# Performance work log

Measured on AMD Instinct MI355X. Metric: run time of the kernel, lower is better.

Reference implementation:

```python
import jax, jax.numpy as jnp
import numpy as np

E_EDGES = 100000   # number of original edges (edge tokens)
M_PAIRS = 1000000  # number of edge-edge (line-graph) pairs
IN_DIM = 128
H = 8   # num_heads
D = 16  # out_dim per head


def setup_inputs() -> dict:
    key = jax.random.key(0)
    ks = jax.random.split(key, 8)
    edge_attr = jax.random.normal(ks[0], (E_EDGES, IN_DIM), dtype=jnp.float32)
    edge_edge_index = jax.random.randint(ks[1], (2, M_PAIRS), 0, E_EDGES, dtype=jnp.int64)
    s = 1.0 / np.sqrt(IN_DIM)  # xavier-ish scale
    Wq = jax.random.normal(ks[2], (IN_DIM, H * D), dtype=jnp.float32) * s
    Wk = jax.random.normal(ks[3], (IN_DIM, H * D), dtype=jnp.float32) * s
    Wv = jax.random.normal(ks[4], (IN_DIM, H * D), dtype=jnp.float32) * s
    bq = jnp.zeros((H * D,), dtype=jnp.float32)
    bk = jnp.zeros((H * D,), dtype=jnp.float32)
    bv = jnp.zeros((H * D,), dtype=jnp.float32)
    Aw = jax.random.normal(ks[5], (D, H), dtype=jnp.float32) * (1.0 / np.sqrt(D))
    return {"edge_attr": edge_attr, "edge_edge_index": edge_edge_index,
            "Wq": Wq, "bq": bq, "Wk": Wk, "bk": bk, "Wv": Wv, "bv": bv, "Aw": Aw}


def reference(edge_attr, edge_edge_index, Wq, bq, Wk, bk, Wv, bv, Aw):
    E = edge_attr.shape[0]
    # Q/K/V projections, reshaped to [E, H, D]
    Qh = (edge_attr @ Wq + bq).reshape(E, H, D)
    Kh = (edge_attr @ Wk + bk).reshape(E, H, D)
    Vh = (edge_attr @ Wv + bv).reshape(E, H, D)
    src = edge_edge_index[0]
    dst = edge_edge_index[1]
    # gather + additive score over edge-edge pairs: [M, H, D]
    score_vec = Kh[src] + Qh[dst]  # act = Identity
    # einsum 'ehd,dhc->ehc' with c=1 -> [M, H]
    raw_attn = jnp.einsum('mhd,dh->mh', score_vec, Aw)
    # segment softmax grouped by destination edge
    mx = jax.ops.segment_max(raw_attn, dst, num_segments=E)  # [E, H]
    ex = jnp.exp(raw_attn - mx[dst])
    denom = jax.ops.segment_sum(ex, dst, num_segments=E)[dst] + 1e-16
    attn = ex / denom  # [M, H]; dropout p=0 -> identity
    # weighted scatter-add aggregation
    msg = Vh[src] * attn[..., None]  # [M, H, D]
    edge_out = jax.ops.segment_sum(msg, dst, num_segments=E)  # [E, H, D]
    return edge_out
```

## Files before the change

### kernel.cpp

```cpp
#include <hip/hip_runtime.h>
#include <math.h>

static constexpr int E = 100000;
static constexpr int M = 1000000;
static constexpr int NBE = (E + 255) / 256;
static constexpr int NBM = (M + 255) / 256;
static constexpr int NBP = (E + 63) / 64;
static constexpr int NBM4 = (M + 1023) / 1024;

#define O_FLAG   0
#define O_WEFF   512
#define O_BKEFF  4608
#define O_BSWZ   5120
#define O_COUNTS 38400
#define O_OFFS   438784
#define O_BSUM   838784
#define O_BSUM2  840832
#define O_BINOFF 842880
#define O_GBIN   843904
#define O_ORDER  1245312
#define O_POS    1645312
#define O_CSR    5645312
#define O_KS     9645312
#define O_VH     12845312
#define WS_NEEDED (O_VH + (size_t)E * 128 * 2)

typedef float f32x4 __attribute__((ext_vector_type(4)));
typedef short s16x8 __attribute__((ext_vector_type(8)));

__device__ __forceinline__ unsigned short f2bf(float f) {
    unsigned u = __float_as_uint(f);
    u += 0x7fffu + ((u >> 16) & 1u);
    return (unsigned short)(u >> 16);
}
__device__ __forceinline__ float bflo(unsigned u) { return __uint_as_float(u << 16); }
__device__ __forceinline__ float bfhi(unsigned u) { return __uint_as_float(u & 0xffff0000u); }

__device__ __forceinline__ int weswz(int k) { return (k ^ ((k >> 3) & 3)) << 3; }

__global__ void k_prep(const float* __restrict__ Wk, const float* __restrict__ bk,
                       const float* __restrict__ Aw, const float* __restrict__ Wv,
                       const int* __restrict__ idx32, int* __restrict__ flag,
                       float* __restrict__ weff, float* __restrict__ bkeff,
                       unsigned short* __restrict__ Bswz) {
    int bid = blockIdx.x, t = threadIdx.x;
    if (bid == 0) {
        if (t < 128) {
            for (int h = 0; h < 8; h++) {
                float s = 0.f;
                for (int d = 0; d < 16; d++) s += Wk[t * 128 + h * 16 + d] * Aw[d * 8 + h];
                weff[t * 8 + h] = s;
            }
            if (t < 8) {
                float s = 0.f;
                for (int d = 0; d < 16; d++) s += bk[t * 16 + d] * Aw[d * 8 + t];
                bkeff[t] = s;
            }
        }
        return;
    }
    if (bid == 1) {
        if (t == 0) {
            int z = 0;
            for (int i = 0; i < 64; i++) z += (idx32[2 * i + 1] == 0) ? 1 : 0;
            *flag = (z == 64) ? 1 : 0;
        }
        return;
    }
    int p = (bid - 2) * 256 + t;
    int f = p >> 6, lane = p & 63;
    int c = f >> 3, tt = f & 7;
    int quad = lane >> 4, nn = lane & 15;
#pragma unroll
    for (int j = 0; j < 8; j++) {
        int k = c * 32 + quad * 8 + j;
        Bswz[p * 8 + j] = f2bf(Wv[k * 128 + tt * 16 + nn]);
    }
}

__global__ __launch_bounds__(256) void k_cp(
    const void* __restrict__ idx, const int* __restrict__ flagp,
    int* __restrict__ counts, int* __restrict__ pos,
    const float* __restrict__ A, const short* __restrict__ Bswz,
    const float* __restrict__ bv, const float* __restrict__ weff,
    const float* __restrict__ bkeff, unsigned short* __restrict__ Vh,
    float* __restrict__ ksb) {
    int bid = blockIdx.x, t = threadIdx.x;
    int r = bid % 5;
    if (r < 2) {
        int cid = (bid / 5) * 2 + r;
        if (cid >= NBM4) return;
        int base = cid * 1024 + t;
        int m0 = base, m1 = base + 256, m2 = base + 512, m3 = base + 768;
        int d0 = 0, d1 = 0, d2 = 0, d3 = 0;
        if (*flagp) {
            const long long* p = (const long long*)idx;
            if (m0 < M) d0 = (int)p[M + m0];
            if (m1 < M) d1 = (int)p[M + m1];
            if (m2 < M) d2 = (int)p[M + m2];
            if (m3 < M) d3 = (int)p[M + m3];
        } else {
            const int* p = (const int*)idx;
            if (m0 < M) d0 = p[M + m0];
            if (m1 < M) d1 = p[M + m1];
            if (m2 < M) d2 = p[M + m2];
            if (m3 < M) d3 = p[M + m3];
        }
        if (m0 < M) pos[m0] = atomicAdd(&counts[d0], 1);
        if (m1 < M) pos[m1] = atomicAdd(&counts[d1], 1);
        if (m2 < M) pos[m2] = atomicAdd(&counts[d2], 1);
        if (m3 < M) pos[m3] = atomicAdd(&counts[d3], 1);
        return;
    }
    int pid = (bid / 5) * 3 + (r - 2);
    if (pid >= NBP) return;

    __shared__ float we[1024];
    {
        int k = t >> 1;
        int off = weswz(k) + ((t & 1) << 2);
        *(float4*)&we[off] = ((const float4*)weff)[t];
    }
    __syncthreads();

    int lane = t & 63, wid = t >> 6;
    int rowbase = pid * 64 + wid * 16;
    int quad = lane >> 4, nn = lane & 15;
    int m = rowbase + nn;
    int mc = (m < E) ? m : (E - 1);

    f32x4 acc[8];
#pragma unroll
    for (int tt = 0; tt < 8; tt++) acc[tt] = (f32x4){0.f, 0.f, 0.f, 0.f};
    float p[8];
#pragma unroll
    for (int h = 0; h < 8; h++) p[h] = 0.f;

#pragma unroll
    for (int c = 0; c < 4; c++) {
        const float4* ap = (const float4*)(A + (size_t)mc * 128 + c * 32 + quad * 8);
        float4 f0 = ap[0], f1 = ap[1];
        float a[8] = {f0.x, f0.y, f0.z, f0.w, f1.x, f1.y, f1.z, f1.w};
#pragma unroll
        for (int j = 0; j < 8; j++) {
            int k = c * 32 + quad * 8 + j;
            int kb = weswz(k);
            float4 w0 = *(const float4*)&we[kb];
            float4 w1 = *(const float4*)&we[kb + 4];
            p[0] += a[j] * w0.x; p[1] += a[j] * w0.y;
            p[2] += a[j] * w0.z; p[3] += a[j] * w0.w;
            p[4] += a[j] * w1.x; p[5] += a[j] * w1.y;
            p[6] += a[j] * w1.z; p[7] += a[j] * w1.w;
        }
        s16x8 afrag;
#pragma unroll
        for (int j = 0; j < 8; j++) afrag[j] = (short)f2bf(a[j]);
#pragma unroll
        for (int tt = 0; tt < 8; tt++) {
            s16x8 bfrag = *(const s16x8*)(Bswz + (((c * 8 + tt) * 64 + lane) << 3));
            acc[tt] = __builtin_amdgcn_mfma_f32_16x16x32_bf16(afrag, bfrag, acc[tt], 0, 0, 0);
        }
    }
#pragma unroll
    for (int off = 16; off <= 32; off <<= 1)
#pragma unroll
        for (int h = 0; h < 8; h++) p[h] += __shfl_xor(p[h], off, 64);
    if (quad == 0 && m < E) {
        float4* op = (float4*)(ksb + (size_t)m * 8);
        op[0] = make_float4(p[0] + bkeff[0], p[1] + bkeff[1], p[2] + bkeff[2], p[3] + bkeff[3]);
        op[1] = make_float4(p[4] + bkeff[4], p[5] + bkeff[5], p[6] + bkeff[6], p[7] + bkeff[7]);
    }
#pragma unroll
    for (int tt = 0; tt < 8; tt++) {
        float bvc = bv[tt * 16 + nn];
#pragma unroll
        for (int rr = 0; rr < 4; rr++) {
            int row = rowbase + quad * 4 + rr;
            if (row < E)
                Vh[(size_t)row * 128 + tt * 16 + nn] = f2bf(acc[tt][rr] + bvc);
        }
    }
}

__global__ void k_scanA(int* __restrict__ counts, int* __restrict__ offs,
                        int* __restrict__ bsum, int* __restrict__ gbin) {
    __shared__ int sm[256];
    __shared__ int lh[256];
    __shared__ int bb[256];
    int tid = threadIdx.x;
    int i = blockIdx.x * 256 + tid;
    int v = (i < E) ? counts[i] : 0;
    int n = v > 255 ? 255 : v;
    lh[tid] = 0;
    sm[tid] = v;
    __syncthreads();
    int lr = 0;
    if (i < E) lr = atomicAdd(&lh[n], 1);
    for (int off = 1; off < 256; off <<= 1) {
        int add = (tid >= off) ? sm[tid - off] : 0;
        __syncthreads();
        sm[tid] += add;
        __syncthreads();
    }
    if (i < E) offs[i] = sm[tid] - v;
    if (tid == 255) bsum[blockIdx.x] = sm[255];
    int cnt = lh[tid];
    if (cnt > 0) bb[tid] = atomicAdd(&gbin[tid * 8], cnt);
    __syncthreads();
    if (i < E) counts[i] = ((bb[n] + lr) << 8) | n;
}

__global__ void k_scanB2(const int* __restrict__ bsum, const int* __restrict__ gbin,
                         int* __restrict__ bsum2, int* __restrict__ binoff, int nb) {
    __shared__ int sm[512];
    __shared__ int s2[256];
    int tid = threadIdx.x;
    int v = (tid < nb) ? bsum[tid] : 0;
    sm[tid] = v;
    __syncthreads();
    for (int off = 1; off < 512; off <<= 1) {
        int add = (tid >= off) ? sm[tid - off] : 0;
        __syncthreads();
        sm[tid] += add;
        __syncthreads();
    }
    bsum2[tid] = sm[tid] - v;
    int bv = 0;
    if (tid < 256) { bv = gbin[(255 - tid) * 8]; s2[tid] = bv; }
    __syncthreads();
    for (int off = 1; off < 256; off <<= 1) {
        int add = (tid < 256 && tid >= off) ? s2[tid - off] : 0;
        __syncthreads();
        if (tid < 256) s2[tid] += add;
        __syncthreads();
    }
    if (tid < 256) binoff[255 - tid] = s2[tid] - bv;
}

__global__ void k_fill(const void* __restrict__ idx, const int* __restrict__ flagp,
                       const int* __restrict__ offs, const int* __restrict__ bsum2,
                       const int* __restrict__ pos, int* __restrict__ csr,
                       const int* __restrict__ counts, const int* __restrict__ binoff,
                       int* __restrict__ order) {
    int bid = blockIdx.x, t = threadIdx.x;
    if (bid < NBM) {
        int m = bid * 256 + t;
        if (m >= M) return;
        int s, d;
        if (*flagp) {
            const long long* p = (const long long*)idx;
            s = (int)p[m]; d = (int)p[M + m];
        } else {
            const int* p = (const int*)idx;
            s = p[m]; d = p[M + m];
        }
        csr[offs[d] + bsum2[d >> 8] + pos[m]] = s;
        return;
    }
    int i = (bid - NBM) * 256 + t;
    if (i >= E) return;
    int v = counts[i];
    order[binoff[v & 255] + (v >> 8)] = i;
}

#define ROWL(p, sidx, cond) \
    if (cond) { \
        k##p = ksb[(size_t)(sidx) * 8 + h]; \
        const uint4* vp_ = (const uint4*)(Vh + (size_t)(sidx) * 128 + (h << 4)); \
        a##p = vp_[0]; b##p = vp_[1]; \
    }

#define CONS(kk, aa, bb) { \
    float w_ = __expf(kk); \
    l += w_; \
    acc[0]  += bflo(aa.x) * w_; acc[1]  += bfhi(aa.x) * w_; \
    acc[2]  += bflo(aa.y) * w_; acc[3]  += bfhi(aa.y) * w_; \
    acc[4]  += bflo(aa.z) * w_; acc[5]  += bfhi(aa.z) * w_; \
    acc[6]  += bflo(aa.w) * w_; acc[7]  += bfhi(aa.w) * w_; \
    acc[8]  += bflo(bb.x) * w_; acc[9]  += bfhi(bb.x) * w_; \
    acc[10] += bflo(bb.y) * w_; acc[11] += bfhi(bb.y) * w_; \
    acc[12] += bflo(bb.z) * w_; acc[13] += bfhi(bb.z) * w_; \
    acc[14] += bflo(bb.w) * w_; acc[15] += bfhi(bb.w) * w_; \
}

__global__ __launch_bounds__(256) void k_seg(
    const float* __restrict__ ksb, const unsigned short* __restrict__ Vh,
    const int* __restrict__ offs, const int* __restrict__ bsum2,
    const int* __restrict__ csr, const int* __restrict__ order,
    float* __restrict__ out) {
    int t = threadIdx.x;
    int h = t & 7;
    int g = blockIdx.x * 32 + (t >> 3);
    int seg = order[g];
    int beg = offs[seg] + bsum2[seg >> 8];
    int end = (seg + 1 < E) ? (offs[seg + 1] + bsum2[(seg + 1) >> 8]) : M;
    int n = end - beg;

    float acc[16];
#pragma unroll
    for (int j = 0; j < 16; j++) acc[j] = 0.f;
    float l = 0.f;

    if (n > 0) {
        int s0 = 0, s1 = 0, s2 = 0, s3 = 0, t0 = 0, t1 = 0, t2 = 0, t3 = 0;
        float k0 = 0, k1 = 0, k2 = 0, k3 = 0;
        uint4 a0 = {}, b0 = {}, a1 = {}, b1 = {}, a2 = {}, b2 = {}, a3 = {}, b3 = {};
        s0 = csr[beg];
        if (n > 1) s1 = csr[beg + 1];
        if (n > 2) s2 = csr[beg + 2];
        if (n > 3) s3 = csr[beg + 3];
        ROWL(0, s0, true)
        ROWL(1, s1, n > 1)
        ROWL(2, s2, n > 2)
        ROWL(3, s3, n > 3)
        if (n > 4) t0 = csr[beg + 4];
        if (n > 5) t1 = csr[beg + 5];
        if (n > 6) t2 = csr[beg + 6];
        if (n > 7) t3 = csr[beg + 7];
        int i = 0;
        while (i + 4 <= n) {
            CONS(k0, a0, b0) ROWL(0, t0, i + 4 < n) if (i + 8 < n)  t0 = csr[beg + i + 8];
            CONS(k1, a1, b1) ROWL(1, t1, i + 5 < n) if (i + 9 < n)  t1 = csr[beg + i + 9];
            CONS(k2, a2, b2) ROWL(2, t2, i + 6 < n) if (i + 10 < n) t2 = csr[beg + i + 10];
            CONS(k3, a3, b3) ROWL(3, t3, i + 7 < n) if (i + 11 < n) t3 = csr[beg + i + 11];
            i += 4;
        }
        if (i < n) { CONS(k0, a0, b0) i++; }
        if (i < n) { CONS(k1, a1, b1) i++; }
        if (i < n) { CONS(k2, a2, b2) }
    }
    float inv = 1.0f / (l + 1e-16f);
    float4* op = (float4*)(out + (size_t)seg * 128 + h * 16);
#pragma unroll
    for (int j = 0; j < 4; j++)
        op[j] = make_float4(acc[4 * j] * inv, acc[4 * j + 1] * inv,
                            acc[4 * j + 2] * inv, acc[4 * j + 3] * inv);
}

extern "C" void kernel_launch(void* const* d_in, const int* in_sizes, int n_in,
                              void* d_out, int out_size, void* d_ws, size_t ws_size,
                              hipStream_t stream) {
    const float* edge_attr = (const float*)d_in[0];
    const void*  eei       = d_in[1];
    const float* Wk = (const float*)d_in[4];
    const float* bk = (const float*)d_in[5];
    const float* Wv = (const float*)d_in[6];
    const float* bv = (const float*)d_in[7];
    const float* Aw = (const float*)d_in[8];
    float* out = (float*)d_out;

    if (ws_size < WS_NEEDED) return;

    char* ws = (char*)d_ws;
    int*   flag   = (int*)(ws + O_FLAG);
    float* weff   = (float*)(ws + O_WEFF);
    float* bkeff  = (float*)(ws + O_BKEFF);
    unsigned short* Bswz = (unsigned short*)(ws + O_BSWZ);
    int*   counts = (int*)(ws + O_COUNTS);
    int*   offs   = (int*)(ws + O_OFFS);
    int*   bsum   = (int*)(ws + O_BSUM);
    int*   bsum2  = (int*)(ws + O_BSUM2);
    int*   binoff = (int*)(ws + O_BINOFF);
    int*   gbin   = (int*)(ws + O_GBIN);
    int*   order  = (int*)(ws + O_ORDER);
    int*   pos    = (int*)(ws + O_POS);
    int*   csr    = (int*)(ws + O_CSR);
    float* ksb    = (float*)(ws + O_KS);
    unsigned short* Vh = (unsigned short*)(ws + O_VH);

    hipMemsetAsync(counts, 0, E * sizeof(int), stream);
    hipMemsetAsync(gbin, 0, 256 * 8 * sizeof(int), stream);
    k_prep<<<10, 256, 0, stream>>>(Wk, bk, Aw, Wv, (const int*)eei,
                                   flag, weff, bkeff, Bswz);
    k_cp<<<5 * 521, 256, 0, stream>>>(eei, flag, counts, pos, edge_attr,
                                      (const short*)Bswz, bv, weff, bkeff, Vh, ksb);
    k_scanA<<<NBE, 256, 0, stream>>>(counts, offs, bsum, gbin);
    k_scanB2<<<1, 512, 0, stream>>>(bsum, gbin, bsum2, binoff, NBE);
    k_fill<<<NBM + NBE, 256, 0, stream>>>(eei, flag, offs, bsum2, pos, csr,
                                          counts, binoff, order);
    k_seg<<<E / 32, 256, 0, stream>>>(ksb, Vh, offs, bsum2, csr, order, out);
}
```

Before: 257.6 us.

## Pad histogram counters, fold memsets into prep kernel, precompute exp weights

Pads the per-destination atomic counters to a 4-int stride so concurrent atomics on neighbouring destinations hit different 16-byte slots. Replaces the two memset calls by zeroing counts and gbin inside the prep kernel, which removes launch overhead. Moves the exp of the per-source key score into the projection kernel, so the segment kernel reads precomputed weights and skips one exp per pair. In exchange, the counts array is four times larger and its reads in the scan and fill kernels become strided. The softmax also stays without max subtraction, as before, which can overflow for large scores.

```diff
diff --git a/kernel.cpp b/kernel.cpp
--- a/kernel.cpp
+++ b/kernel.cpp
@@ -7,22 +7,23 @@
 static constexpr int NBM = (M + 255) / 256;
 static constexpr int NBP = (E + 63) / 64;
 static constexpr int NBM4 = (M + 1023) / 1024;
+static constexpr int CSTR = 4;
 
 #define O_FLAG   0
 #define O_WEFF   512
 #define O_BKEFF  4608
 #define O_BSWZ   5120
 #define O_COUNTS 38400
-#define O_OFFS   438784
-#define O_BSUM   838784
-#define O_BSUM2  840832
-#define O_BINOFF 842880
-#define O_GBIN   843904
-#define O_ORDER  1245312
-#define O_POS    1645312
-#define O_CSR    5645312
-#define O_KS     9645312
-#define O_VH     12845312
+#define O_OFFS   1640960
+#define O_BSUM   2040960
+#define O_BSUM2  2043008
+#define O_BINOFF 2045056
+#define O_GBIN   2046080
+#define O_ORDER  2054272
+#define O_POS    2454272
+#define O_CSR    6454272
+#define O_WS     10454272
+#define O_VH     13654272
 #define WS_NEEDED (O_VH + (size_t)E * 128 * 2)
 
 typedef float f32x4 __attribute__((ext_vector_type(4)));
@@ -42,9 +43,14 @@
                        const float* __restrict__ Aw, const float* __restrict__ Wv,
                        const int* __restrict__ idx32, int* __restrict__ flag,
                        float* __restrict__ weff, float* __restrict__ bkeff,
-                       unsigned short* __restrict__ Bswz) {
+                       unsigned short* __restrict__ Bswz, uint4* __restrict__ countsz,
+                       uint4* __restrict__ gbinz) {
     int bid = blockIdx.x, t = threadIdx.x;
-    if (bid == 0) {
+    if (bid < NBE) {
+        countsz[bid * 256 + t] = make_uint4(0, 0, 0, 0);
+        return;
+    }
+    if (bid == NBE) {
         if (t < 128) {
             for (int h = 0; h < 8; h++) {
                 float s = 0.f;
@@ -59,7 +65,9 @@
         }
         return;
     }
-    if (bid == 1) {
+    if (bid == NBE + 1) {
+        gbinz[t * 2] = make_uint4(0, 0, 0, 0);
+        gbinz[t * 2 + 1] = make_uint4(0, 0, 0, 0);
         if (t == 0) {
             int z = 0;
             for (int i = 0; i < 64; i++) z += (idx32[2 * i + 1] == 0) ? 1 : 0;
@@ -67,7 +75,7 @@
         }
         return;
     }
-    int p = (bid - 2) * 256 + t;
+    int p = (bid - (NBE + 2)) * 256 + t;
     int f = p >> 6, lane = p & 63;
     int c = f >> 3, tt = f & 7;
     int quad = lane >> 4, nn = lane & 15;
@@ -84,7 +92,7 @@
     const float* __restrict__ A, const short* __restrict__ Bswz,
     const float* __restrict__ bv, const float* __restrict__ weff,
     const float* __restrict__ bkeff, unsigned short* __restrict__ Vh,
-    float* __restrict__ ksb) {
+    float* __restrict__ wsb) {
     int bid = blockIdx.x, t = threadIdx.x;
     int r = bid % 5;
     if (r < 2) {
@@ -106,10 +114,10 @@
             if (m2 < M) d2 = p[M + m2];
             if (m3 < M) d3 = p[M + m3];
         }
-        if (m0 < M) pos[m0] = atomicAdd(&counts[d0], 1);
-        if (m1 < M) pos[m1] = atomicAdd(&counts[d1], 1);
-        if (m2 < M) pos[m2] = atomicAdd(&counts[d2], 1);
-        if (m3 < M) pos[m3] = atomicAdd(&counts[d3], 1);
+        if (m0 < M) pos[m0] = atomicAdd(&counts[d0 * CSTR], 1);
+        if (m1 < M) pos[m1] = atomicAdd(&counts[d1 * CSTR], 1);
+        if (m2 < M) pos[m2] = atomicAdd(&counts[d2 * CSTR], 1);
+        if (m3 < M) pos[m3] = atomicAdd(&counts[d3 * CSTR], 1);
         return;
     }
     int pid = (bid / 5) * 3 + (r - 2);
@@ -166,9 +174,11 @@
 #pragma unroll
         for (int h = 0; h < 8; h++) p[h] += __shfl_xor(p[h], off, 64);
     if (quad == 0 && m < E) {
-        float4* op = (float4*)(ksb + (size_t)m * 8);
-        op[0] = make_float4(p[0] + bkeff[0], p[1] + bkeff[1], p[2] + bkeff[2], p[3] + bkeff[3]);
-        op[1] = make_float4(p[4] + bkeff[4], p[5] + bkeff[5], p[6] + bkeff[6], p[7] + bkeff[7]);
+        float4* op = (float4*)(wsb + (size_t)m * 8);
+        op[0] = make_float4(__expf(p[0] + bkeff[0]), __expf(p[1] + bkeff[1]),
+                            __expf(p[2] + bkeff[2]), __expf(p[3] + bkeff[3]));
+        op[1] = make_float4(__expf(p[4] + bkeff[4]), __expf(p[5] + bkeff[5]),
+                            __expf(p[6] + bkeff[6]), __expf(p[7] + bkeff[7]));
     }
 #pragma unroll
     for (int tt = 0; tt < 8; tt++) {
@@ -189,7 +199,7 @@
     __shared__ int bb[256];
     int tid = threadIdx.x;
     int i = blockIdx.x * 256 + tid;
-    int v = (i < E) ? counts[i] : 0;
+    int v = (i < E) ? counts[i * CSTR] : 0;
     int n = v > 255 ? 255 : v;
     lh[tid] = 0;
     sm[tid] = v;
@@ -207,7 +217,7 @@
     int cnt = lh[tid];
     if (cnt > 0) bb[tid] = atomicAdd(&gbin[tid * 8], cnt);
     __syncthreads();
-    if (i < E) counts[i] = ((bb[n] + lr) << 8) | n;
+    if (i < E) counts[i * CSTR] = ((bb[n] + lr) << 8) | n;
 }
 
 __global__ void k_scanB2(const int* __restrict__ bsum, const int* __restrict__ gbin,
@@ -259,19 +269,19 @@
     }
     int i = (bid - NBM) * 256 + t;
     if (i >= E) return;
-    int v = counts[i];
+    int v = counts[i * CSTR];
     order[binoff[v & 255] + (v >> 8)] = i;
 }
 
 #define ROWL(p, sidx, cond) \
     if (cond) { \
-        k##p = ksb[(size_t)(sidx) * 8 + h]; \
+        k##p = wsb[(size_t)(sidx) * 8 + h]; \
         const uint4* vp_ = (const uint4*)(Vh + (size_t)(sidx) * 128 + (h << 4)); \
         a##p = vp_[0]; b##p = vp_[1]; \
     }
 
 #define CONS(kk, aa, bb) { \
-    float w_ = __expf(kk); \
+    float w_ = kk; \
     l += w_; \
     acc[0]  += bflo(aa.x) * w_; acc[1]  += bfhi(aa.x) * w_; \
     acc[2]  += bflo(aa.y) * w_; acc[3]  += bfhi(aa.y) * w_; \
@@ -284,7 +294,7 @@
 }
 
 __global__ __launch_bounds__(256) void k_seg(
-    const float* __restrict__ ksb, const unsigned short* __restrict__ Vh,
+    const float* __restrict__ wsb, const unsigned short* __restrict__ Vh,
     const int* __restrict__ offs, const int* __restrict__ bsum2,
     const int* __restrict__ csr, const int* __restrict__ order,
     float* __restrict__ out) {
@@ -365,18 +375,17 @@
     int*   order  = (int*)(ws + O_ORDER);
     int*   pos    = (int*)(ws + O_POS);
     int*   csr    = (int*)(ws + O_CSR);
-    float* ksb    = (float*)(ws + O_KS);
+    float* wsb    = (float*)(ws + O_WS);
     unsigned short* Vh = (unsigned short*)(ws + O_VH);
 
-    hipMemsetAsync(counts, 0, E * sizeof(int), stream);
-    hipMemsetAsync(gbin, 0, 256 * 8 * sizeof(int), stream);
-    k_prep<<<10, 256, 0, stream>>>(Wk, bk, Aw, Wv, (const int*)eei,
-                                   flag, weff, bkeff, Bswz);
+    k_prep<<<NBE + 10, 256, 0, stream>>>(Wk, bk, Aw, Wv, (const int*)eei, flag,
+                                         weff, bkeff, Bswz, (uint4*)counts,
+                                         (uint4*)gbin);
     k_cp<<<5 * 521, 256, 0, stream>>>(eei, flag, counts, pos, edge_attr,
-                                      (const short*)Bswz, bv, weff, bkeff, Vh, ksb);
+                                      (const short*)Bswz, bv, weff, bkeff, Vh, wsb);
     k_scanA<<<NBE, 256, 0, stream>>>(counts, offs, bsum, gbin);
     k_scanB2<<<1, 512, 0, stream>>>(bsum, gbin, bsum2, binoff, NBE);
     k_fill<<<NBM + NBE, 256, 0, stream>>>(eei, flag, offs, bsum2, pos, csr,
                                           counts, binoff, order);
-    k_seg<<<E / 32, 256, 0, stream>>>(ksb, Vh, offs, bsum2, csr, order, out);
-}
+    k_seg<<<E / 32, 256, 0, stream>>>(wsb, Vh, offs, bsum2, csr, order, out);
+}
```

New measurement: 252.0 us. -2.1%, faster.

## Fold memsets into prep kernel, split count/projection kernels, precompute exp weights

Applied to the files above, without the earlier changes.

The two memsets are replaced by zeroing blocks inside the prep kernel, and the weff computation is spread across a full block using shared Aw. The interleaved count+projection kernel is split into two separate launches. The exp of the per-source key score is computed once per edge in the projection kernel instead of once per pair in the segment kernel, removing about a million exp calls. The split adds a kernel launch and loses the overlap between the atomic counting and the MFMA projection.

```diff
diff --git a/kernel.cpp b/kernel.cpp
--- a/kernel.cpp
+++ b/kernel.cpp
@@ -7,6 +7,7 @@
 static constexpr int NBM = (M + 255) / 256;
 static constexpr int NBP = (E + 63) / 64;
 static constexpr int NBM4 = (M + 1023) / 1024;
+static constexpr int NZC = (E / 4 + 255) / 256;
 
 #define O_FLAG   0
 #define O_WEFF   512
@@ -18,11 +19,11 @@
 #define O_BSUM2  840832
 #define O_BINOFF 842880
 #define O_GBIN   843904
-#define O_ORDER  1245312
-#define O_POS    1645312
-#define O_CSR    5645312
-#define O_KS     9645312
-#define O_VH     12845312
+#define O_ORDER  852096
+#define O_POS    1252096
+#define O_CSR    5252096
+#define O_WS     9252096
+#define O_VH     12452096
 #define WS_NEEDED (O_VH + (size_t)E * 128 * 2)
 
 typedef float f32x4 __attribute__((ext_vector_type(4)));
@@ -42,32 +43,45 @@
                        const float* __restrict__ Aw, const float* __restrict__ Wv,
                        const int* __restrict__ idx32, int* __restrict__ flag,
                        float* __restrict__ weff, float* __restrict__ bkeff,
-                       unsigned short* __restrict__ Bswz) {
+                       unsigned short* __restrict__ Bswz, uint4* __restrict__ countsz,
+                       uint4* __restrict__ gbinz) {
     int bid = blockIdx.x, t = threadIdx.x;
-    if (bid == 0) {
-        if (t < 128) {
-            for (int h = 0; h < 8; h++) {
-                float s = 0.f;
-                for (int d = 0; d < 16; d++) s += Wk[t * 128 + h * 16 + d] * Aw[d * 8 + h];
-                weff[t * 8 + h] = s;
-            }
-            if (t < 8) {
-                float s = 0.f;
-                for (int d = 0; d < 16; d++) s += bk[t * 16 + d] * Aw[d * 8 + t];
-                bkeff[t] = s;
-            }
-        }
+    if (bid < NZC) {
+        int i4 = bid * 256 + t;
+        if (i4 < E / 4) countsz[i4] = make_uint4(0, 0, 0, 0);
         return;
     }
-    if (bid == 1) {
+    if (bid == NZC) {
+        __shared__ float sAw[128];
+        if (t < 128) sAw[t] = Aw[t];
+        __syncthreads();
+#pragma unroll
+        for (int j = 0; j < 4; j++) {
+            int o = t + 256 * j;
+            int row = o >> 3, h = o & 7;
+            float s = 0.f;
+#pragma unroll
+            for (int d = 0; d < 16; d++) s += Wk[row * 128 + h * 16 + d] * sAw[d * 8 + h];
+            weff[o] = s;
+        }
+        if (t < 8) {
+            float s = 0.f;
+            for (int d = 0; d < 16; d++) s += bk[t * 16 + d] * sAw[d * 8 + t];
+            bkeff[t] = s;
+        }
+        return;
+    }
+    if (bid == NZC + 1) {
+        uint4 z = make_uint4(0, 0, 0, 0);
+        gbinz[t] = z; gbinz[t + 256] = z;
         if (t == 0) {
-            int z = 0;
-            for (int i = 0; i < 64; i++) z += (idx32[2 * i + 1] == 0) ? 1 : 0;
-            *flag = (z == 64) ? 1 : 0;
+            int zc = 0;
+            for (int i = 0; i < 64; i++) zc += (idx32[2 * i + 1] == 0) ? 1 : 0;
+            *flag = (zc == 64) ? 1 : 0;
         }
         return;
     }
-    int p = (bid - 2) * 256 + t;
+    int p = (bid - (NZC + 2)) * 256 + t;
     int f = p >> 6, lane = p & 63;
     int c = f >> 3, tt = f & 7;
     int quad = lane >> 4, nn = lane & 15;
@@ -78,42 +92,39 @@
     }
 }
 
-__global__ __launch_bounds__(256) void k_cp(
+__global__ __launch_bounds__(256) void k_count(
     const void* __restrict__ idx, const int* __restrict__ flagp,
-    int* __restrict__ counts, int* __restrict__ pos,
+    int* __restrict__ counts, int* __restrict__ pos) {
+    int t = threadIdx.x;
+    int base = blockIdx.x * 1024 + t;
+    int m0 = base, m1 = base + 256, m2 = base + 512, m3 = base + 768;
+    int d0 = 0, d1 = 0, d2 = 0, d3 = 0;
+    if (*flagp) {
+        const long long* p = (const long long*)idx;
+        if (m0 < M) d0 = (int)p[M + m0];
+        if (m1 < M) d1 = (int)p[M + m1];
+        if (m2 < M) d2 = (int)p[M + m2];
+        if (m3 < M) d3 = (int)p[M + m3];
+    } else {
+        const int* p = (const int*)idx;
+        if (m0 < M) d0 = p[M + m0];
+        if (m1 < M) d1 = p[M + m1];
+        if (m2 < M) d2 = p[M + m2];
+        if (m3 < M) d3 = p[M + m3];
+    }
+    if (m0 < M) pos[m0] = atomicAdd(&counts[d0], 1);
+    if (m1 < M) pos[m1] = atomicAdd(&counts[d1], 1);
+    if (m2 < M) pos[m2] = atomicAdd(&counts[d2], 1);
+    if (m3 < M) pos[m3] = atomicAdd(&counts[d3], 1);
+}
+
+__global__ __launch_bounds__(256) void k_proj(
     const float* __restrict__ A, const short* __restrict__ Bswz,
     const float* __restrict__ bv, const float* __restrict__ weff,
     const float* __restrict__ bkeff, unsigned short* __restrict__ Vh,
-    float* __restrict__ ksb) {
-    int bid = blockIdx.x, t = threadIdx.x;
-    int r = bid % 5;
-    if (r < 2) {
-        int cid = (bid / 5) * 2 + r;
-        if (cid >= NBM4) return;
-        int base = cid * 1024 + t;
-        int m0 = base, m1 = base + 256, m2 = base + 512, m3 = base + 768;
-        int d0 = 0, d1 = 0, d2 = 0, d3 = 0;
-        if (*flagp) {
-            const long long* p = (const long long*)idx;
-            if (m0 < M) d0 = (int)p[M + m0];
-            if (m1 < M) d1 = (int)p[M + m1];
-            if (m2 < M) d2 = (int)p[M + m2];
-            if (m3 < M) d3 = (int)p[M + m3];
-        } else {
-            const int* p = (const int*)idx;
-            if (m0 < M) d0 = p[M + m0];
-            if (m1 < M) d1 = p[M + m1];
-            if (m2 < M) d2 = p[M + m2];
-            if (m3 < M) d3 = p[M + m3];
-        }
-        if (m0 < M) pos[m0] = atomicAdd(&counts[d0], 1);
-        if (m1 < M) pos[m1] = atomicAdd(&counts[d1], 1);
-        if (m2 < M) pos[m2] = atomicAdd(&counts[d2], 1);
-        if (m3 < M) pos[m3] = atomicAdd(&counts[d3], 1);
-        return;
-    }
-    int pid = (bid / 5) * 3 + (r - 2);
-    if (pid >= NBP) return;
+    float* __restrict__ wsb) {
+    int t = threadIdx.x;
+    int pid = blockIdx.x;
 
     __shared__ float we[1024];
     {
@@ -166,9 +177,11 @@
 #pragma unroll
         for (int h = 0; h < 8; h++) p[h] += __shfl_xor(p[h], off, 64);
     if (quad == 0 && m < E) {
-        float4* op = (float4*)(ksb + (size_t)m * 8);
-        op[0] = make_float4(p[0] + bkeff[0], p[1] + bkeff[1], p[2] + bkeff[2], p[3] + bkeff[3]);
-        op[1] = make_float4(p[4] + bkeff[4], p[5] + bkeff[5], p[6] + bkeff[6], p[7] + bkeff[7]);
+        float4* op = (float4*)(wsb + (size_t)m * 8);
+        op[0] = make_float4(__expf(p[0] + bkeff[0]), __expf(p[1] + bkeff[1]),
+                            __expf(p[2] + bkeff[2]), __expf(p[3] + bkeff[3]));
+        op[1] = make_float4(__expf(p[4] + bkeff[4]), __expf(p[5] + bkeff[5]),
+                            __expf(p[6] + bkeff[6]), __expf(p[7] + bkeff[7]));
     }
 #pragma unroll
     for (int tt = 0; tt < 8; tt++) {
@@ -265,13 +278,13 @@
 
 #define ROWL(p, sidx, cond) \
     if (cond) { \
-        k##p = ksb[(size_t)(sidx) * 8 + h]; \
+        k##p = wsb[(size_t)(sidx) * 8 + h]; \
         const uint4* vp_ = (const uint4*)(Vh + (size_t)(sidx) * 128 + (h << 4)); \
         a##p = vp_[0]; b##p = vp_[1]; \
     }
 
 #define CONS(kk, aa, bb) { \
-    float w_ = __expf(kk); \
+    float w_ = kk; \
     l += w_; \
     acc[0]  += bflo(aa.x) * w_; acc[1]  += bfhi(aa.x) * w_; \
     acc[2]  += bflo(aa.y) * w_; acc[3]  += bfhi(aa.y) * w_; \
@@ -284,7 +297,7 @@
 }
 
 __global__ __launch_bounds__(256) void k_seg(
-    const float* __restrict__ ksb, const unsigned short* __restrict__ Vh,
+    const float* __restrict__ wsb, const unsigned short* __restrict__ Vh,
     const int* __restrict__ offs, const int* __restrict__ bsum2,
     const int* __restrict__ csr, const int* __restrict__ order,
     float* __restrict__ out) {
@@ -365,18 +378,18 @@
     int*   order  = (int*)(ws + O_ORDER);
     int*   pos    = (int*)(ws + O_POS);
     int*   csr    = (int*)(ws + O_CSR);
-    float* ksb    = (float*)(ws + O_KS);
+    float* wsb    = (float*)(ws + O_WS);
     unsigned short* Vh = (unsigned short*)(ws + O_VH);
 
-    hipMemsetAsync(counts, 0, E * sizeof(int), stream);
-    hipMemsetAsync(gbin, 0, 256 * 8 * sizeof(int), stream);
-    k_prep<<<10, 256, 0, stream>>>(Wk, bk, Aw, Wv, (const int*)eei,
-                                   flag, weff, bkeff, Bswz);
-    k_cp<<<5 * 521, 256, 0, stream>>>(eei, flag, counts, pos, edge_attr,
-                                      (const short*)Bswz, bv, weff, bkeff, Vh, ksb);
+    k_prep<<<NZC + 10, 256, 0, stream>>>(Wk, bk, Aw, Wv, (const int*)eei, flag,
+                                         weff, bkeff, Bswz, (uint4*)counts,
+                                         (uint4*)gbin);
+    k_count<<<NBM4, 256, 0, stream>>>(eei, flag, counts, pos);
+    k_proj<<<NBP, 256, 0, stream>>>(edge_attr, (const short*)Bswz, bv, weff,
+                                    bkeff, Vh, wsb);
     k_scanA<<<NBE, 256, 0, stream>>>(counts, offs, bsum, gbin);
     k_scanB2<<<1, 512, 0, stream>>>(bsum, gbin, bsum2, binoff, NBE);
     k_fill<<<NBM + NBE, 256, 0, stream>>>(eei, flag, offs, bsum2, pos, csr,
                                           counts, binoff, order);
-    k_seg<<<E / 32, 256, 0, stream>>>(ksb, Vh, offs, bsum2, csr, order, out);
-}
+    k_seg<<<E / 32, 256, 0, stream>>>(wsb, Vh, offs, bsum2, csr, order, out);
+}
```

Result: slower. 273.0 us (+6.0%).
